# Optimization experiments

Hardware: AMD Instinct MI355X
Metric: run time of the kernel (lower is better)

## Reference

```python
import jax, jax.numpy as jnp
import numpy as np

N, C, H, W = 4, 128, 64, 64
HEADS, KS, RED = 4, 7, 18
D = C // HEADS


def _layernorm(x, w, b, eps=1e-5):
    mu = x.mean(axis=-1, keepdims=True)
    var = ((x - mu) ** 2).mean(axis=-1, keepdims=True)
    return (x - mu) * jax.lax.rsqrt(var + eps) * w + b


def _gelu(x):
    return jax.nn.gelu(x, approximate=False)


def setup_inputs() -> dict:
    key = jax.random.key(0)
    ks = jax.random.split(key, 16)
    s = 0.02
    inp = {
        'x': jax.random.normal(ks[0], (N, C, H, W), jnp.float32),
        'ln1_w': jnp.ones((C,), jnp.float32), 'ln1_b': jnp.zeros((C,), jnp.float32),
        'ln2_w': jnp.ones((C,), jnp.float32), 'ln2_b': jnp.zeros((C,), jnp.float32),
        'qkv_w': jax.random.normal(ks[1], (C, 3 * C), jnp.float32) * s,
        'qkv_b': jnp.zeros((3 * C,), jnp.float32),
        'proj_w': jax.random.normal(ks[2], (C, C), jnp.float32) * s,
        'proj_b': jnp.zeros((C,), jnp.float32),
        'rpb': jax.random.normal(ks[3], (HEADS, 2 * KS - 1, 2 * KS - 1), jnp.float32) * s,
        'conv1_w': jax.random.normal(ks[4], (C, C // 4), jnp.float32) * s,
        'conv1_b': jnp.zeros((C // 4,), jnp.float32),
        'conv2_w': jax.random.normal(ks[5], (C // 4, C), jnp.float32) * s,
        'conv2_b': jnp.zeros((C,), jnp.float32),
        'ca1_w': jax.random.normal(ks[6], (C, C // RED), jnp.float32) * s,
        'ca1_b': jnp.zeros((C // RED,), jnp.float32),
        'ca2_w': jax.random.normal(ks[7], (C // RED, C), jnp.float32) * s,
        'ca2_b': jnp.zeros((C,), jnp.float32),
        'fc1_w': jax.random.normal(ks[8], (C, 4 * C), jnp.float32) * s,
        'fc1_b': jnp.zeros((4 * C,), jnp.float32),
        'fc2_w': jax.random.normal(ks[9], (4 * C, C), jnp.float32) * s,
        'fc2_b': jnp.zeros((C,), jnp.float32),
    }
    return inp


def _na2d(xc, qkv_w, qkv_b, rpb, proj_w, proj_b):
    # xc: [N, H, W, C] -> neighborhood attention with clamped k x k windows (NATTEN semantics)
    n, h, w, c = xc.shape
    qkv = (xc @ qkv_w + qkv_b).reshape(n, h, w, 3, HEADS, D)
    q, k, v = qkv[..., 0, :, :], qkv[..., 1, :, :], qkv[..., 2, :, :]
    q = q * (D ** -0.5)
    half = KS // 2
    ni = jnp.clip(jnp.arange(h) - half, 0, h - KS)          # window start per query row
    nj = jnp.clip(jnp.arange(w) - half, 0, w - KS)
    idx_i = ni[:, None] + jnp.arange(KS)                     # [H, KS]
    idx_j = nj[:, None] + jnp.arange(KS)                     # [W, KS]
    # gather key/value windows: [N, H, KS, W, KS, heads, D]
    kw = k[:, idx_i][:, :, :, idx_j]
    vw = v[:, idx_i][:, :, :, idx_j]
    attn = jnp.einsum('nijhd,niajbhd->nijhab', q, kw)        # [N,H,W,heads,KS,KS]
    bi = idx_i - jnp.arange(h)[:, None] + (KS - 1)           # rel-pos bias row index [H,KS]
    bj = idx_j - jnp.arange(w)[:, None] + (KS - 1)           # [W,KS]
    bias = rpb[:, bi][:, :, :, bj]                           # [heads,H,KS,W,KS]
    attn = attn + bias.transpose(1, 3, 0, 2, 4)[None]        # -> [1,H,W,heads,KS,KS]
    attn = jax.nn.softmax(attn.reshape(n, h, w, HEADS, KS * KS), axis=-1)
    attn = attn.reshape(n, h, w, HEADS, KS, KS)
    out = jnp.einsum('nijhab,niajbhd->nijhd', attn, vw).reshape(n, h, w, c)
    return out @ proj_w + proj_b


def reference(x, ln1_w, ln1_b, ln2_w, ln2_b, qkv_w, qkv_b, proj_w, proj_b, rpb,
              conv1_w, conv1_b, conv2_w, conv2_b, ca1_w, ca1_b, ca2_w, ca2_b,
              fc1_w, fc1_b, fc2_w, fc2_b):
    n, c, h, w = x.shape
    xs = x.transpose(0, 2, 3, 1).reshape(n, h * w, c)        # n (h w) c
    shortcut = xs
    xn = _layernorm(xs, ln1_w, ln1_b)
    xc = xn.reshape(n, h, w, c)
    # conv branch: 1x1 -> GELU -> 1x1 -> channel attention
    t = _gelu(xc @ conv1_w + conv1_b) @ conv2_w + conv2_b
    g = t.mean(axis=(1, 2))                                  # global avg pool [N,C]
    g = jax.nn.sigmoid(jax.nn.relu(g @ ca1_w + ca1_b) @ ca2_w + ca2_b)
    ca_x = (t * g[:, None, None, :]).reshape(n, h * w, c)
    # neighborhood attention branch
    na_x = _na2d(xc, qkv_w, qkv_b, rpb, proj_w, proj_b).reshape(n, h * w, c)
    x2 = shortcut + na_x + ca_x * 0.02
    m = _gelu(_layernorm(x2, ln2_w, ln2_b) @ fc1_w + fc1_b) @ fc2_w + fc2_b
    x3 = x2 + m
    return x3.reshape(n, h, w, c).transpose(0, 3, 1, 2)
```

## Files before the change

### kernel.cpp

```cpp
#include <hip/hip_runtime.h>
#include <hip/hip_bf16.h>
#include <math.h>

#define NB 4
#define CC 128
#define HH 64
#define WW 64
#define HEADS 4
#define KS 7
#define DD 32
#define HW 4096
#define MTOT 16384

typedef unsigned short BF;
typedef short short8 __attribute__((ext_vector_type(8)));
typedef float floatx4 __attribute__((ext_vector_type(4)));

__device__ __forceinline__ float gelu_f(float x) {
    return 0.5f * x * (1.0f + erff(x * 0.70710678118654752440f));
}

__device__ __forceinline__ BF f2bf(float f) {
    union { float f; unsigned u; } a; a.f = f;
    unsigned u = a.u;
    unsigned r = u + 0x7FFFu + ((u >> 16) & 1u);
    return (BF)(r >> 16);
}

__device__ __forceinline__ float bf2f(BF v) {
    return __uint_as_float(((unsigned)v) << 16);
}

#define LDK 40
#define LDK128 136

__global__ __launch_bounds__(256) void ln1t_kernel(
    const float* __restrict__ x, const float* __restrict__ w,
    const float* __restrict__ b, BF* __restrict__ out,
    float* __restrict__ part)
{
    __shared__ float xt[128][33];
    __shared__ float mus[32], rss[32];
    const int blk = blockIdx.x;
    const int n  = blk >> 7;
    const int p0 = (blk & 127) * 32;
    const int t  = threadIdx.x;
    if (blk < 4 && t < 128) part[blk * CC + t] = 0.f;

    {
        int pp = t & 31, c8 = t >> 5;
        #pragma unroll 4
        for (int it = 0; it < 16; it++) {
            int c = it * 8 + c8;
            xt[c][pp] = x[(size_t)(n * CC + c) * HW + p0 + pp];
        }
    }
    __syncthreads();
    {
        int pp2 = t >> 3, cb = t & 7;
        float s = 0.f;
        #pragma unroll
        for (int u = 0; u < 16; u++) s += xt[cb + u * 8][pp2];
        s += __shfl_xor(s, 1); s += __shfl_xor(s, 2); s += __shfl_xor(s, 4);
        float mu = s * (1.0f / CC);
        float v = 0.f;
        #pragma unroll
        for (int u = 0; u < 16; u++) { float d = xt[cb + u * 8][pp2] - mu; v += d * d; }
        v += __shfl_xor(v, 1); v += __shfl_xor(v, 2); v += __shfl_xor(v, 4);
        if (cb == 0) { mus[pp2] = mu; rss[pp2] = rsqrtf(v * (1.0f / CC) + 1e-5f); }
    }
    __syncthreads();
    {
        #pragma unroll
        for (int it = 0; it < 2; it++) {
            int pp2 = (t >> 4) + it * 16;
            int c0  = (t & 15) * 8;
            float mu = mus[pp2], rs = rss[pp2];
            int m = n * HW + p0 + pp2;
            short8 o;
            #pragma unroll
            for (int u = 0; u < 8; u++)
                o[u] = (short)f2bf((xt[c0 + u][pp2] - mu) * rs * w[c0 + u] + b[c0 + u]);
            *(short8*)(out + (size_t)m * CC + c0) = o;
        }
    }
}

template<int ACT>
__device__ __forceinline__ void k128_body(
    const BF* __restrict__ A, const float* __restrict__ B,
    const float* __restrict__ bias, BF* __restrict__ Cout,
    int N, int row0, int col0, BF* Bl )
{
    const int t = threadIdx.x;
    const int w = t >> 6, lane = t & 63, q = lane >> 4, r16 = lane & 15;
    {
        int kk = t >> 1, nn0 = (t & 1) * 32;
        const float* src = B + (size_t)kk * N + col0 + nn0;
        #pragma unroll
        for (int u = 0; u < 32; u++) Bl[(nn0 + u) * LDK128 + kk] = f2bf(src[u]);
    }
    __syncthreads();
    floatx4 acc[4] = {};
    const BF* arow = A + (size_t)(row0 + w * 16 + r16) * CC;
    #pragma unroll
    for (int ks = 0; ks < 4; ks++) {
        short8 af = *(const short8*)(arow + ks * 32 + q * 8);
        #pragma unroll
        for (int nt = 0; nt < 4; nt++) {
            short8 bf = *(const short8*)(Bl + (nt * 16 + r16) * LDK128 + ks * 32 + q * 8);
            acc[nt] = __builtin_amdgcn_mfma_f32_16x16x32_bf16(af, bf, acc[nt], 0, 0, 0);
        }
    }
    #pragma unroll
    for (int nt = 0; nt < 4; nt++) {
        int col = col0 + nt * 16 + r16;
        float bv = bias[col];
        #pragma unroll
        for (int reg = 0; reg < 4; reg++) {
            int row = row0 + w * 16 + q * 4 + reg;
            float v = acc[nt][reg] + bv;
            if (ACT == 1) v = gelu_f(v);
            Cout[(size_t)row * N + col] = f2bf(v);
        }
    }
}

__global__ __launch_bounds__(256) void phase2(
    const BF* __restrict__ xn, const float* __restrict__ qkv_w,
    const float* __restrict__ qkv_b, BF* __restrict__ qkv_out,
    const float* __restrict__ w1, const float* __restrict__ b1,
    const float* __restrict__ w2, const float* __restrict__ b2,
    BF* __restrict__ tout, float* __restrict__ part)
{
    __shared__ __align__(16) char smem[26624];
    const int bid = blockIdx.x;
    const int t = threadIdx.x;
    const int w = t >> 6, lane = t & 63, q = lane >> 4, r16 = lane & 15;

    if (bid < 1536) {
        int col0 = (bid % 6) * 64;
        int row0 = (bid / 6) * 64;
        k128_body<0>(xn, qkv_w, qkv_b, qkv_out, 384, row0, col0, (BF*)smem);
        return;
    }
    BF*    W1l = (BF*)smem;
    BF*    W2l = (BF*)(smem + 8704);
    BF*    Hl  = (BF*)(smem + 18944);
    float* red = (float*)(smem + 24064);
    const int row0 = (bid - 1536) * 64;
    {
        int kk = t >> 1, nn = (t & 1) * 16;
        const float* src = w1 + (size_t)kk * 32 + nn;
        #pragma unroll
        for (int u = 0; u < 16; u++) W1l[(nn + u) * LDK128 + kk] = f2bf(src[u]);
    }
    {
        int kk = t >> 3, n0 = (t & 7) * 16;
        const float* src = w2 + (size_t)kk * 128 + n0;
        #pragma unroll
        for (int u = 0; u < 16; u++) W2l[(n0 + u) * LDK + kk] = f2bf(src[u]);
    }
    __syncthreads();
    floatx4 a1[2] = {};
    const BF* arow = xn + (size_t)(row0 + w * 16 + r16) * CC;
    #pragma unroll
    for (int ks = 0; ks < 4; ks++) {
        short8 af = *(const short8*)(arow + ks * 32 + q * 8);
        #pragma unroll
        for (int nt = 0; nt < 2; nt++) {
            short8 bf = *(const short8*)(W1l + (nt * 16 + r16) * LDK128 + ks * 32 + q * 8);
            a1[nt] = __builtin_amdgcn_mfma_f32_16x16x32_bf16(af, bf, a1[nt], 0, 0, 0);
        }
    }
    #pragma unroll
    for (int nt = 0; nt < 2; nt++) {
        int col = nt * 16 + r16;
        float bv = b1[col];
        #pragma unroll
        for (int reg = 0; reg < 4; reg++)
            Hl[(w * 16 + q * 4 + reg) * LDK + col] = f2bf(gelu_f(a1[nt][reg] + bv));
    }
    __syncthreads();
    floatx4 a2[8] = {};
    short8 af2 = *(const short8*)(Hl + (w * 16 + r16) * LDK + q * 8);
    #pragma unroll
    for (int nt = 0; nt < 8; nt++) {
        short8 bf = *(const short8*)(W2l + (nt * 16 + r16) * LDK + q * 8);
        a2[nt] = __builtin_amdgcn_mfma_f32_16x16x32_bf16(af2, bf, a2[nt], 0, 0, 0);
    }
    #pragma unroll
    for (int nt = 0; nt < 8; nt++) {
        int col = nt * 16 + r16;
        float bv = b2[col];
        float s = 0.f;
        #pragma unroll
        for (int reg = 0; reg < 4; reg++) {
            int row = row0 + w * 16 + q * 4 + reg;
            float v = a2[nt][reg] + bv;
            tout[(size_t)row * CC + col] = f2bf(v);
            s += v;
        }
        s += __shfl_xor(s, 16);
        s += __shfl_xor(s, 32);
        if (lane < 16) red[w * 128 + col] = s;
    }
    __syncthreads();
    if (t < 128) {
        float cs = red[t] + red[128 + t] + red[256 + t] + red[384 + t];
        atomicAdd(&part[(row0 >> 12) * CC + t], cs);
    }
}

template<int ACT>
__global__ __launch_bounds__(256) void gemm_k128(
    const BF* __restrict__ A, const float* __restrict__ B,
    const float* __restrict__ bias, BF* __restrict__ Cout, int N)
{
    __shared__ __align__(16) BF Bl[64 * LDK128];
    k128_body<ACT>(A, B, bias, Cout, N, blockIdx.y * 64, blockIdx.x * 64, Bl);
}

__global__ __launch_bounds__(256) void na_mfma_kernel(
    const BF* __restrict__ qkv, const float* __restrict__ rpb,
    BF* __restrict__ outp)
{
    __shared__ __align__(16) BF Kt[224][40];
    __shared__ __align__(16) BF Vt[32][232];
    __shared__ __align__(16) BF Qb[64][40];
    __shared__ __align__(16) BF Pl[4][16][232];
    __shared__ float rb[169];

    const int b = blockIdx.x;
    const int h = b & 3;
    const int tile = b >> 2;
    const int n = tile >> 6;
    const int ti = (tile >> 3) & 7, tj = tile & 7;
    const int t = threadIdx.x;
    const int w = t >> 6, lane = t & 63, quad = lane >> 4, r16 = lane & 15;
    const int i0 = ti * 8, j0 = tj * 8;
    const int wi0 = max(i0 - 3, 0), wj0 = max(j0 - 3, 0);
    const int R  = min(wi0 + 13, 63) - wi0 + 1;
    const int Rj = min(wj0 + 13, 63) - wj0 + 1;

    for (int idx = t; idx < 896; idx += 256) {
        int key = idx >> 2, ch = idx & 3;
        int kr = key >> 4, kc = key & 15;
        uint4 v = {0u, 0u, 0u, 0u};
        if (kr < R && kc < Rj) {
            size_t pix = (size_t)((n * HH + wi0 + kr) * WW + wj0 + kc);
            v = *(const uint4*)(qkv + pix * 384 + 128 + h * DD + ch * 8);
        }
        *(uint4*)&Kt[key][ch * 8] = v;
    }
    for (int idx = t; idx < 896; idx += 256) {
        int key = idx >> 2, ch = idx & 3;
        int kr = key >> 4, kc = key & 15;
        if (kr < R && kc < Rj) {
            size_t pix = (size_t)((n * HH + wi0 + kr) * WW + wj0 + kc);
            uint4 v = *(const uint4*)(qkv + pix * 384 + 256 + h * DD + ch * 8);
            const BF* pv = (const BF*)&v;
            #pragma unroll
            for (int u = 0; u < 8; u++) Vt[ch * 8 + u][key] = pv[u];
        } else {
            #pragma unroll
            for (int u = 0; u < 8; u++) Vt[ch * 8 + u][key] = 0;
        }
    }
    {
        int q = t >> 2, ch = t & 3;
        size_t mq = (size_t)((n * HH + i0 + (q >> 3)) * WW + j0 + (q & 7));
        *(uint4*)&Qb[q][ch * 8] = *(const uint4*)(qkv + mq * 384 + h * DD + ch * 8);
    }
    if (t < 169) rb[t] = rpb[h * 169 + t];
    __syncthreads();

    int oi[4], cok[4], bj0[4], ai_[4];
    #pragma unroll
    for (int reg = 0; reg < 4; reg++) {
        int q = w * 16 + quad * 4 + reg;
        int i = i0 + (q >> 3), j = j0 + (q & 7);
        int ni = min(max(i - 3, 0), HH - KS), nj = min(max(j - 3, 0), WW - KS);
        oi[reg]  = ni - wi0;
        ai_[reg] = ni - i + 6;
        int dc = r16 - (nj - wj0);
        cok[reg] = ((unsigned)dc < 7u) ? 1 : 0;
        bj0[reg] = min(max(dc + (nj - j + 6), 0), 12);
    }

    short8 aq = *(const short8*)&Qb[w * 16 + r16][quad * 8];
    floatx4 S[14];
    #pragma unroll
    for (int nt = 0; nt < 14; nt++) {
        floatx4 z = {0.f, 0.f, 0.f, 0.f};
        short8 bk = *(const short8*)&Kt[nt * 16 + r16][quad * 8];
        S[nt] = __builtin_amdgcn_mfma_f32_16x16x32_bf16(aq, bk, z, 0, 0, 0);
    }
    const float scale = 0.17677669529663688110f;
    #pragma unroll
    for (int nt = 0; nt < 14; nt++) {
        #pragma unroll
        for (int reg = 0; reg < 4; reg++) {
            int dr = nt - oi[reg];
            bool ok = ((unsigned)dr < 7u) && cok[reg];
            int bi = min(max(dr + ai_[reg], 0), 12);
            float bias = rb[bi * 13 + bj0[reg]];
            S[nt][reg] = ok ? fmaf(S[nt][reg], scale, bias) : -1e30f;
        }
    }
    float rinv[4];
    #pragma unroll
    for (int reg = 0; reg < 4; reg++) {
        float m = S[0][reg];
        #pragma unroll
        for (int nt = 1; nt < 14; nt++) m = fmaxf(m, S[nt][reg]);
        m = fmaxf(m, __shfl_xor(m, 1));
        m = fmaxf(m, __shfl_xor(m, 2));
        m = fmaxf(m, __shfl_xor(m, 4));
        m = fmaxf(m, __shfl_xor(m, 8));
        float s = 0.f;
        #pragma unroll
        for (int nt = 0; nt < 14; nt++) {
            float e = __expf(S[nt][reg] - m);
            S[nt][reg] = e;
            s += e;
        }
        s += __shfl_xor(s, 1);
        s += __shfl_xor(s, 2);
        s += __shfl_xor(s, 4);
        s += __shfl_xor(s, 8);
        rinv[reg] = 1.0f / s;
    }
    #pragma unroll
    for (int nt = 0; nt < 14; nt++)
        #pragma unroll
        for (int reg = 0; reg < 4; reg++)
            Pl[w][quad * 4 + reg][nt * 16 + r16] = f2bf(S[nt][reg] * rinv[reg]);

    floatx4 O0 = {0.f, 0.f, 0.f, 0.f}, O1 = {0.f, 0.f, 0.f, 0.f};
    #pragma unroll
    for (int ks = 0; ks < 7; ks++) {
        short8 ap = *(const short8*)&Pl[w][r16][ks * 32 + quad * 8];
        short8 b0 = *(const short8*)&Vt[r16][ks * 32 + quad * 8];
        short8 b1 = *(const short8*)&Vt[16 + r16][ks * 32 + quad * 8];
        O0 = __builtin_amdgcn_mfma_f32_16x16x32_bf16(ap, b0, O0, 0, 0, 0);
        O1 = __builtin_amdgcn_mfma_f32_16x16x32_bf16(ap, b1, O1, 0, 0, 0);
    }
    #pragma unroll
    for (int reg = 0; reg < 4; reg++) {
        int q = w * 16 + quad * 4 + reg;
        size_t m = (size_t)((n * HH + i0 + (q >> 3)) * WW + j0 + (q & 7));
        outp[m * CC + h * DD + r16]      = f2bf(O0[reg]);
        outp[m * CC + h * DD + 16 + r16] = f2bf(O1[reg]);
    }
}

__global__ __launch_bounds__(256) void projx2ln2g(
    const BF* __restrict__ A, const float* __restrict__ Bw,
    const float* __restrict__ bias, const float* __restrict__ x,
    const BF* __restrict__ tbuf, const float* __restrict__ part,
    const float* __restrict__ ca1_w, const float* __restrict__ ca1_b,
    const float* __restrict__ ca2_w, const float* __restrict__ ca2_b,
    const float* __restrict__ w2, const float* __restrict__ b2,
    float* __restrict__ x2b, BF* __restrict__ lnout)
{
    __shared__ __align__(16) BF Bl[128 * LDK128];
    __shared__ float xs[64][132];
    __shared__ float gs[128];
    __shared__ float h1[7];
    __shared__ float gl[128];

    const int t = threadIdx.x;
    const int w = t >> 6, lane = t & 63, q = lane >> 4, r16 = lane & 15;
    const int row0 = blockIdx.x * 64;
    const int n = row0 >> 12;
    const int p0 = row0 & 4095;

    {
        int kk = t >> 1, nn0 = (t & 1) * 64;
        const float* src = Bw + (size_t)kk * CC + nn0;
        #pragma unroll
        for (int u = 0; u < 64; u++) Bl[(nn0 + u) * LDK128 + kk] = f2bf(src[u]);
    }
    {
        #pragma unroll
        for (int it = 0; it < 8; it++) {
            int idx4 = it * 256 + t;
            int p4 = idx4 & 15, c = idx4 >> 4;
            float4 v = *(const float4*)(x + (size_t)(n * CC + c) * HW + p0 + p4 * 4);
            xs[p4 * 4 + 0][c] = v.x; xs[p4 * 4 + 1][c] = v.y;
            xs[p4 * 4 + 2][c] = v.z; xs[p4 * 4 + 3][c] = v.w;
        }
    }
    if (t < 128) gs[t] = part[n * CC + t] * (1.0f / HW);
    __syncthreads();
    if (t < 7) {
        float a = ca1_b[t];
        for (int k = 0; k < 128; k++) a += gs[k] * ca1_w[k * 7 + t];
        h1[t] = fmaxf(a, 0.f);
    }
    __syncthreads();
    if (t < 128) {
        float o = ca2_b[t];
        #pragma unroll
        for (int r = 0; r < 7; r++) o += h1[r] * ca2_w[r * 128 + t];
        gl[t] = 1.0f / (1.0f + expf(-o));
    }

    floatx4 acc[8] = {};
    const BF* arow = A + (size_t)(row0 + w * 16 + r16) * CC;
    #pragma unroll
    for (int ks = 0; ks < 4; ks++) {
        short8 af = *(const short8*)(arow + ks * 32 + q * 8);
        #pragma unroll
        for (int nt = 0; nt < 8; nt++) {
            short8 bf = *(const short8*)(Bl + (nt * 16 + r16) * LDK128 + ks * 32 + q * 8);
            acc[nt] = __builtin_amdgcn_mfma_f32_16x16x32_bf16(af, bf, acc[nt], 0, 0, 0);
        }
    }
    __syncthreads();

    float s1[4] = {0.f, 0.f, 0.f, 0.f}, s2[4] = {0.f, 0.f, 0.f, 0.f};
    #pragma unroll
    for (int nt = 0; nt < 8; nt++) {
        int col = nt * 16 + r16;
        float bv = bias[col];
        float gv = gl[col];
        #pragma unroll
        for (int reg = 0; reg < 4; reg++) {
            int lr = w * 16 + q * 4 + reg;
            int row = row0 + lr;
            float xv = xs[lr][col];
            float tv = bf2f(tbuf[(size_t)row * CC + col]);
            float v = acc[nt][reg] + bv + xv + 0.02f * tv * gv;
            acc[nt][reg] = v;
            s1[reg] += v;
            s2[reg] += v * v;
        }
    }
    #pragma unroll
    for (int reg = 0; reg < 4; reg++) {
        #pragma unroll
        for (int off = 8; off; off >>= 1) {
            s1[reg] += __shfl_xor(s1[reg], off);
            s2[reg] += __shfl_xor(s2[reg], off);
        }
    }
    float mu[4], rr[4];
    #pragma unroll
    for (int reg = 0; reg < 4; reg++) {
        mu[reg] = s1[reg] * (1.0f / CC);
        float var = s2[reg] * (1.0f / CC) - mu[reg] * mu[reg];
        rr[reg] = rsqrtf(var + 1e-5f);
    }
    #pragma unroll
    for (int nt = 0; nt < 8; nt++) {
        int col = nt * 16 + r16;
        float wv = w2[col], bv2 = b2[col];
        #pragma unroll
        for (int reg = 0; reg < 4; reg++) {
            int row = row0 + w * 16 + q * 4 + reg;
            float v = acc[nt][reg];
            x2b[(size_t)row * CC + col] = v;
            lnout[(size_t)row * CC + col] = f2bf((v - mu[reg]) * rr[reg] * wv + bv2);
        }
    }
}

__global__ __launch_bounds__(256) void fc2_kernel(
    const BF* __restrict__ A, const float* __restrict__ B,
    const float* __restrict__ bias, const float* __restrict__ x2b,
    float* __restrict__ out)
{
    __shared__ __align__(16) BF Alds[64][LDK];
    __shared__ __align__(16) BF Blds[64][LDK];
    __shared__ float st[64][66];

    const int t    = threadIdx.x;
    const int w    = t >> 6;
    const int lane = t & 63;
    const int q    = lane >> 4;
    const int r16  = lane & 15;
    const int row0 = blockIdx.y * 64;
    const int col0 = blockIdx.x * 64;
    const int n    = row0 >> 12;
    const int p0   = row0 & 4095;

    floatx4 acc[4] = {};
    const int ar = t >> 2;
    const int ak = (t & 3) * 8;
    const int bk = t >> 3;
    const int bn = (t & 7) * 8;

    for (int k0 = 0; k0 < 512; k0 += 32) {
        *(short8*)(&Alds[ar][ak]) =
            *(const short8*)(A + (size_t)(row0 + ar) * 512 + k0 + ak);
        {
            const float* src = B + (size_t)(k0 + bk) * CC + col0 + bn;
            float4 b0 = *(const float4*)(src);
            float4 b1 = *(const float4*)(src + 4);
            Blds[bn + 0][bk] = f2bf(b0.x); Blds[bn + 1][bk] = f2bf(b0.y);
            Blds[bn + 2][bk] = f2bf(b0.z); Blds[bn + 3][bk] = f2bf(b0.w);
            Blds[bn + 4][bk] = f2bf(b1.x); Blds[bn + 5][bk] = f2bf(b1.y);
            Blds[bn + 6][bk] = f2bf(b1.z); Blds[bn + 7][bk] = f2bf(b1.w);
        }
        __syncthreads();
        short8 af = *(const short8*)(&Alds[w * 16 + r16][q * 8]);
        short8 bfm[4];
        #pragma unroll
        for (int nt = 0; nt < 4; nt++)
            bfm[nt] = *(const short8*)(&Blds[nt * 16 + r16][q * 8]);
        #pragma unroll
        for (int nt = 0; nt < 4; nt++)
            acc[nt] = __builtin_amdgcn_mfma_f32_16x16x32_bf16(af, bfm[nt], acc[nt], 0, 0, 0);
        __syncthreads();
    }

    #pragma unroll
    for (int nt = 0; nt < 4; nt++) {
        int col = col0 + nt * 16 + r16;
        float bv = bias[col];
        #pragma unroll
        for (int reg = 0; reg < 4; reg++) {
            int lr = w * 16 + q * 4 + reg;
            int row = row0 + lr;
            st[nt * 16 + r16][lr] = acc[nt][reg] + bv + x2b[(size_t)row * CC + col];
        }
    }
    __syncthreads();
    {
        int cc = t >> 2, ch = (t & 3) * 16;
        float* dst = out + (size_t)(n * CC + col0 + cc) * HW + p0 + ch;
        #pragma unroll
        for (int u = 0; u < 4; u++) {
            float4 v;
            v.x = st[cc][ch + u * 4 + 0];
            v.y = st[cc][ch + u * 4 + 1];
            v.z = st[cc][ch + u * 4 + 2];
            v.w = st[cc][ch + u * 4 + 3];
            *(float4*)(dst + u * 4) = v;
        }
    }
}

extern "C" void kernel_launch(void* const* d_in, const int* in_sizes, int n_in,
                              void* d_out, int out_size, void* d_ws, size_t ws_size,
                              hipStream_t stream)
{
    const float* x       = (const float*)d_in[0];
    const float* ln1_w   = (const float*)d_in[1];
    const float* ln1_b   = (const float*)d_in[2];
    const float* ln2_w   = (const float*)d_in[3];
    const float* ln2_b   = (const float*)d_in[4];
    const float* qkv_w   = (const float*)d_in[5];
    const float* qkv_b   = (const float*)d_in[6];
    const float* proj_w  = (const float*)d_in[7];
    const float* proj_b  = (const float*)d_in[8];
    const float* rpb     = (const float*)d_in[9];
    const float* conv1_w = (const float*)d_in[10];
    const float* conv1_b = (const float*)d_in[11];
    const float* conv2_w = (const float*)d_in[12];
    const float* conv2_b = (const float*)d_in[13];
    const float* ca1_w   = (const float*)d_in[14];
    const float* ca1_b   = (const float*)d_in[15];
    const float* ca2_w   = (const float*)d_in[16];
    const float* ca2_b   = (const float*)d_in[17];
    const float* fc1_w   = (const float*)d_in[18];
    const float* fc1_b   = (const float*)d_in[19];
    const float* fc2_w   = (const float*)d_in[20];
    const float* fc2_b   = (const float*)d_in[21];
    float* out = (float*)d_out;

    char* ws = (char*)d_ws;
    BF*    xn_bf   = (BF*)(ws);
    BF*    qkv_bf  = (BF*)(ws + 4194304);
    BF*    hbuf_bf = (BF*)(ws);
    BF*    t_bf    = (BF*)(ws + 16777216);
    float* x2b     = (float*)(ws + 25165824);
    BF*    na_bf   = (BF*)(ws + 33554432);
    BF*    ln2_bf  = (BF*)(ws + 37748736);
    float* part    = (float*)(ws + 41943040);

    ln1t_kernel<<<512, 256, 0, stream>>>(x, ln1_w, ln1_b, xn_bf, part);
    phase2<<<1792, 256, 0, stream>>>(xn_bf, qkv_w, qkv_b, qkv_bf,
                                     conv1_w, conv1_b, conv2_w, conv2_b, t_bf, part);
    na_mfma_kernel<<<1024, 256, 0, stream>>>(qkv_bf, rpb, na_bf);
    projx2ln2g<<<256, 256, 0, stream>>>(na_bf, proj_w, proj_b, x, t_bf, part,
                                        ca1_w, ca1_b, ca2_w, ca2_b,
                                        ln2_w, ln2_b, x2b, ln2_bf);
    gemm_k128<1><<<dim3(8, 256), 256, 0, stream>>>(ln2_bf, fc1_w, fc1_b, hbuf_bf, 512);
    fc2_kernel<<<dim3(2, 256), 256, 0, stream>>>(hbuf_bf, fc2_w, fc2_b, x2b, out);
}
```

Measured before the change: 193.3 us.

## Pre-transpose and convert all weights to bf16 once in the LN1 kernel

Adds 128 extra blocks to the first kernel that convert every GEMM weight matrix into a transposed bf16 copy in workspace, once per call. Downstream GEMM kernels then load the weights with vector copies straight into LDS instead of each block reading fp32, converting and doing scattered transposed LDS stores. This removes redundant conversion work and strided stores repeated across thousands of blocks. The cost is extra workspace traffic and a conversion pass whose global reads in the first kernel are strided and uncoalesced.

New measurement: 174.6 us. 1.11x faster.

```diff
diff --git a/kernel.cpp b/kernel.cpp
--- a/kernel.cpp
+++ b/kernel.cpp
@@ -37,14 +37,45 @@
 __global__ __launch_bounds__(256) void ln1t_kernel(
     const float* __restrict__ x, const float* __restrict__ w,
     const float* __restrict__ b, BF* __restrict__ out,
-    float* __restrict__ part)
-{
+    float* __restrict__ part,
+    const float* __restrict__ qkv_w, const float* __restrict__ conv1_w,
+    const float* __restrict__ conv2_w, const float* __restrict__ proj_w,
+    const float* __restrict__ fc1_w, const float* __restrict__ fc2_w,
+    BF* __restrict__ qkvT, BF* __restrict__ c1T, BF* __restrict__ c2T,
+    BF* __restrict__ projT, BF* __restrict__ fc1T, BF* __restrict__ fc2T)
+{
+    const int blk = blockIdx.x;
+    const int t  = threadIdx.x;
+
+    if (blk >= 512) {
+        for (int idx = (blk - 512) * 256 + t; idx < 204800; idx += 32768) {
+            if (idx < 49152) {
+                int l = idx, n = l >> 7, k = l & 127;
+                qkvT[l] = f2bf(qkv_w[k * 384 + n]);
+            } else if (idx < 53248) {
+                int l = idx - 49152, n = l >> 7, k = l & 127;
+                c1T[l] = f2bf(conv1_w[k * 32 + n]);
+            } else if (idx < 57344) {
+                int l = idx - 53248, n = l >> 5, k = l & 31;
+                c2T[l] = f2bf(conv2_w[k * 128 + n]);
+            } else if (idx < 73728) {
+                int l = idx - 57344, n = l >> 7, k = l & 127;
+                projT[l] = f2bf(proj_w[k * 128 + n]);
+            } else if (idx < 139264) {
+                int l = idx - 73728, n = l >> 7, k = l & 127;
+                fc1T[l] = f2bf(fc1_w[k * 512 + n]);
+            } else {
+                int l = idx - 139264, n = l >> 9, k = l & 511;
+                fc2T[l] = f2bf(fc2_w[k * 128 + n]);
+            }
+        }
+        return;
+    }
+
     __shared__ float xt[128][33];
     __shared__ float mus[32], rss[32];
-    const int blk = blockIdx.x;
     const int n  = blk >> 7;
     const int p0 = (blk & 127) * 32;
-    const int t  = threadIdx.x;
     if (blk < 4 && t < 128) part[blk * CC + t] = 0.f;
 
     {
@@ -88,17 +119,19 @@
 
 template<int ACT>
 __device__ __forceinline__ void k128_body(
-    const BF* __restrict__ A, const float* __restrict__ B,
+    const BF* __restrict__ A, const BF* __restrict__ Bt,
     const float* __restrict__ bias, BF* __restrict__ Cout,
     int N, int row0, int col0, BF* Bl )
 {
     const int t = threadIdx.x;
     const int w = t >> 6, lane = t & 63, q = lane >> 4, r16 = lane & 15;
     {
-        int kk = t >> 1, nn0 = (t & 1) * 32;
-        const float* src = B + (size_t)kk * N + col0 + nn0;
-        #pragma unroll
-        for (int u = 0; u < 32; u++) Bl[(nn0 + u) * LDK128 + kk] = f2bf(src[u]);
+        int nn = t >> 2;
+        int kk = (t & 3) * 32;
+        const BF* src = Bt + (size_t)(col0 + nn) * 128 + kk;
+        #pragma unroll
+        for (int u = 0; u < 4; u++)
+            *(uint4*)(Bl + nn * LDK128 + kk + u * 8) = *(const uint4*)(src + u * 8);
     }
     __syncthreads();
     floatx4 acc[4] = {};
@@ -127,10 +160,10 @@
 }
 
 __global__ __launch_bounds__(256) void phase2(
-    const BF* __restrict__ xn, const float* __restrict__ qkv_w,
+    const BF* __restrict__ xn, const BF* __restrict__ qkvT,
     const float* __restrict__ qkv_b, BF* __restrict__ qkv_out,
-    const float* __restrict__ w1, const float* __restrict__ b1,
-    const float* __restrict__ w2, const float* __restrict__ b2,
+    const BF* __restrict__ c1T, const float* __restrict__ b1,
+    const BF* __restrict__ c2T, const float* __restrict__ b2,
     BF* __restrict__ tout, float* __restrict__ part)
 {
     __shared__ __align__(16) char smem[26624];
@@ -141,7 +174,7 @@
     if (bid < 1536) {
         int col0 = (bid % 6) * 64;
         int row0 = (bid / 6) * 64;
-        k128_body<0>(xn, qkv_w, qkv_b, qkv_out, 384, row0, col0, (BF*)smem);
+        k128_body<0>(xn, qkvT, qkv_b, qkv_out, 384, row0, col0, (BF*)smem);
         return;
     }
     BF*    W1l = (BF*)smem;
@@ -150,16 +183,20 @@
     float* red = (float*)(smem + 24064);
     const int row0 = (bid - 1536) * 64;
     {
-        int kk = t >> 1, nn = (t & 1) * 16;
-        const float* src = w1 + (size_t)kk * 32 + nn;
-        #pragma unroll
-        for (int u = 0; u < 16; u++) W1l[(nn + u) * LDK128 + kk] = f2bf(src[u]);
-    }
-    {
-        int kk = t >> 3, n0 = (t & 7) * 16;
-        const float* src = w2 + (size_t)kk * 128 + n0;
-        #pragma unroll
-        for (int u = 0; u < 16; u++) W2l[(n0 + u) * LDK + kk] = f2bf(src[u]);
+        #pragma unroll
+        for (int it = 0; it < 2; it++) {
+            int idx = it * 256 + t;
+            int nn = idx >> 4, u = idx & 15;
+            *(uint4*)(W1l + nn * LDK128 + u * 8) = *(const uint4*)(c1T + nn * 128 + u * 8);
+        }
+    }
+    {
+        #pragma unroll
+        for (int it = 0; it < 2; it++) {
+            int idx = it * 256 + t;
+            int nn = idx >> 2, u = idx & 3;
+            *(uint4*)(W2l + nn * LDK + u * 8) = *(const uint4*)(c2T + nn * 32 + u * 8);
+        }
     }
     __syncthreads();
     floatx4 a1[2] = {};
@@ -214,11 +251,11 @@
 
 template<int ACT>
 __global__ __launch_bounds__(256) void gemm_k128(
-    const BF* __restrict__ A, const float* __restrict__ B,
+    const BF* __restrict__ A, const BF* __restrict__ Bt,
     const float* __restrict__ bias, BF* __restrict__ Cout, int N)
 {
     __shared__ __align__(16) BF Bl[64 * LDK128];
-    k128_body<ACT>(A, B, bias, Cout, N, blockIdx.y * 64, blockIdx.x * 64, Bl);
+    k128_body<ACT>(A, Bt, bias, Cout, N, blockIdx.y * 64, blockIdx.x * 64, Bl);
 }
 
 __global__ __launch_bounds__(256) void na_mfma_kernel(
@@ -356,7 +393,7 @@
 }
 
 __global__ __launch_bounds__(256) void projx2ln2g(
-    const BF* __restrict__ A, const float* __restrict__ Bw,
+    const BF* __restrict__ A, const BF* __restrict__ projT,
     const float* __restrict__ bias, const float* __restrict__ x,
     const BF* __restrict__ tbuf, const float* __restrict__ part,
     const float* __restrict__ ca1_w, const float* __restrict__ ca1_b,
@@ -377,10 +414,12 @@
     const int p0 = row0 & 4095;
 
     {
-        int kk = t >> 1, nn0 = (t & 1) * 64;
-        const float* src = Bw + (size_t)kk * CC + nn0;
-        #pragma unroll
-        for (int u = 0; u < 64; u++) Bl[(nn0 + u) * LDK128 + kk] = f2bf(src[u]);
+        #pragma unroll
+        for (int it = 0; it < 8; it++) {
+            int idx = it * 256 + t;
+            int nn = idx >> 4, u = idx & 15;
+            *(uint4*)(Bl + nn * LDK128 + u * 8) = *(const uint4*)(projT + nn * 128 + u * 8);
+        }
     }
     {
         #pragma unroll
@@ -468,7 +507,7 @@
 }
 
 __global__ __launch_bounds__(256) void fc2_kernel(
-    const BF* __restrict__ A, const float* __restrict__ B,
+    const BF* __restrict__ A, const BF* __restrict__ fc2T,
     const float* __restrict__ bias, const float* __restrict__ x2b,
     float* __restrict__ out)
 {
@@ -489,21 +528,14 @@
     floatx4 acc[4] = {};
     const int ar = t >> 2;
     const int ak = (t & 3) * 8;
-    const int bk = t >> 3;
-    const int bn = (t & 7) * 8;
+    const int bnn = t >> 2;
+    const int bko = (t & 3) * 8;
 
     for (int k0 = 0; k0 < 512; k0 += 32) {
         *(short8*)(&Alds[ar][ak]) =
             *(const short8*)(A + (size_t)(row0 + ar) * 512 + k0 + ak);
-        {
-            const float* src = B + (size_t)(k0 + bk) * CC + col0 + bn;
-            float4 b0 = *(const float4*)(src);
-            float4 b1 = *(const float4*)(src + 4);
-            Blds[bn + 0][bk] = f2bf(b0.x); Blds[bn + 1][bk] = f2bf(b0.y);
-            Blds[bn + 2][bk] = f2bf(b0.z); Blds[bn + 3][bk] = f2bf(b0.w);
-            Blds[bn + 4][bk] = f2bf(b1.x); Blds[bn + 5][bk] = f2bf(b1.y);
-            Blds[bn + 6][bk] = f2bf(b1.z); Blds[bn + 7][bk] = f2bf(b1.w);
-        }
+        *(uint4*)(&Blds[bnn][bko]) =
+            *(const uint4*)(fc2T + (size_t)(col0 + bnn) * 512 + k0 + bko);
         __syncthreads();
         short8 af = *(const short8*)(&Alds[w * 16 + r16][q * 8]);
         short8 bfm[4];
@@ -580,14 +612,22 @@
     BF*    na_bf   = (BF*)(ws + 33554432);
     BF*    ln2_bf  = (BF*)(ws + 37748736);
     float* part    = (float*)(ws + 41943040);
-
-    ln1t_kernel<<<512, 256, 0, stream>>>(x, ln1_w, ln1_b, xn_bf, part);
-    phase2<<<1792, 256, 0, stream>>>(xn_bf, qkv_w, qkv_b, qkv_bf,
-                                     conv1_w, conv1_b, conv2_w, conv2_b, t_bf, part);
+    BF*    qkvT    = (BF*)(ws + 41945088);
+    BF*    c1T     = (BF*)(ws + 42043392);
+    BF*    c2T     = (BF*)(ws + 42051584);
+    BF*    projT   = (BF*)(ws + 42059776);
+    BF*    fc1T    = (BF*)(ws + 42092544);
+    BF*    fc2T    = (BF*)(ws + 42223616);
+
+    ln1t_kernel<<<640, 256, 0, stream>>>(x, ln1_w, ln1_b, xn_bf, part,
+        qkv_w, conv1_w, conv2_w, proj_w, fc1_w, fc2_w,
+        qkvT, c1T, c2T, projT, fc1T, fc2T);
+    phase2<<<1792, 256, 0, stream>>>(xn_bf, qkvT, qkv_b, qkv_bf,
+                                     c1T, conv1_b, c2T, conv2_b, t_bf, part);
     na_mfma_kernel<<<1024, 256, 0, stream>>>(qkv_bf, rpb, na_bf);
-    projx2ln2g<<<256, 256, 0, stream>>>(na_bf, proj_w, proj_b, x, t_bf, part,
+    projx2ln2g<<<256, 256, 0, stream>>>(na_bf, projT, proj_b, x, t_bf, part,
                                         ca1_w, ca1_b, ca2_w, ca2_b,
                                         ln2_w, ln2_b, x2b, ln2_bf);
-    gemm_k128<1><<<dim3(8, 256), 256, 0, stream>>>(ln2_bf, fc1_w, fc1_b, hbuf_bf, 512);
-    fc2_kernel<<<dim3(2, 256), 256, 0, stream>>>(hbuf_bf, fc2_w, fc2_b, x2b, out);
-}
+    gemm_k128<1><<<dim3(8, 256), 256, 0, stream>>>(ln2_bf, fc1T, fc1_b, hbuf_bf, 512);
+    fc2_kernel<<<dim3(2, 256), 256, 0, stream>>>(hbuf_bf, fc2T, fc2_b, x2b, out);
+}
```
